# Kernel tuning notes

Hardware: AMD Instinct MI355X
Metric: run time of the kernel (lower is better)

Reference implementation:

```python
import jax, jax.numpy as jnp
import numpy as np

M, N = 63, 127            # parity checks x code length (BCH(127,64))
B = 256                   # base batch of codewords
NUM_SHIFTS = 4            # GL 'num_shifts'
NUM_ITERS = 3             # GL 'num_iterations'
PENALTY = 2.0             # GL 'penalty_weight'
BIG = 1e30

_POS = (2 * np.arange(N)) % N          # Frobenius automorphism i -> 2i mod n
_INV = np.zeros(N, np.int32); _INV[_POS] = np.arange(N)
_STEP = N // NUM_SHIFTS
_SHIFTS = [i * _STEP for i in range(NUM_SHIFTS)]  # deterministic (offset=0)


def setup_inputs() -> dict:
    key = jax.random.key(0)
    k1, k2 = jax.random.split(key)
    soft_input = jax.random.normal(k1, (B, N), dtype=jnp.float32)
    labels = jax.random.randint(k2, (B, N), 0, 2).astype(jnp.int32)
    rng = np.random.default_rng(0)
    Hnp = (rng.random((M, N)) < 0.25).astype(np.float32)
    rows = np.arange(M)
    Hnp[rows, rows % N] = 1.0              # guarantee >=2 ones per check row
    Hnp[rows, (rows + 1) % N] = 1.0
    H = jnp.asarray(Hnp, jnp.float32)
    check_weight = jnp.array([0.421], jnp.float32)
    return {"soft_input": soft_input, "labels": labels, "H": H,
            "check_weight": check_weight}


def _interleave(a, b):
    m, n1 = a.shape
    n2 = b.shape[1]
    if n1 == n2:
        return jnp.stack([a, b], axis=2).reshape(m, n1 + n2)
    inter = jnp.stack([a[:, :n2], b], axis=2).reshape(m, 2 * n2)
    return jnp.concatenate([inter, a[:, n2:]], axis=1)


def _compute_cv(vc, H, check_weight):
    # vc: [Bs, M, N] masked variable->check messages
    sign = jnp.sign((1.0 - H)[None] + vc)
    row_sign = jnp.prod(sign, axis=2, keepdims=True)      # product over row
    result_sign = row_sign * H * sign                     # extrinsic sign
    back = jnp.where(H == 0, -BIG - 1.0, 0.0)[None]
    vabs = jnp.clip(jnp.abs(vc), 0.0, BIG)
    top2 = jax.lax.top_k(-vabs + back, 2)[0]              # [Bs, M, 2]
    min1 = -top2[..., 0:1] * H                            # per-check min
    min2 = -top2[..., 1:2] * H                            # per-check 2nd min
    result = jnp.where(vabs > min1, min1, min2)           # extrinsic min
    return jax.nn.softplus(check_weight) * result * jax.lax.stop_gradient(result_sign)


def _iteration(soft, H, check_weight):
    # build super batch: [orig ; even/odd split ; frobenius perm] x rolled copies
    split = jnp.concatenate([soft[:, 0::2], soft[:, 1::2]], axis=1)
    perm = soft[:, _POS]
    base = jnp.concatenate([soft, split, perm], axis=0)   # [3B, N]
    sup = jnp.concatenate([jnp.roll(base, s, axis=1) for s in _SHIFTS], axis=0)
    vc = sup[:, None, :] * H[None]                        # [3B*S, M, N]
    cv = _compute_cv(vc, H, check_weight)
    temp = jnp.sum(cv, axis=1)                            # [3B*S, N]
    bs = 3 * B
    chunks = [jnp.roll(temp[i * bs:(i + 1) * bs], -_SHIFTS[i], axis=1)
              for i in range(NUM_SHIFTS)]
    t1 = sum(c[:B] for c in chunks)
    t2 = sum(c[B:2 * B] for c in chunks)
    width = (N + 1) // 2
    inter = _interleave(t2[:, :width], t2[:, width:])
    t3 = sum(c[2 * B:] for c in chunks)
    p = t3[:, _INV]                                       # inverse Frobenius
    return soft + (t1 + inter + p) / (3.0 * NUM_SHIFTS)


def _loss(soft, labels_f):
    weight = jnp.where(jnp.sign(soft) != 1.0 - 2.0 * labels_f, PENALTY, 1.0)
    z = -soft
    ce = jnp.maximum(z, 0.0) - z * labels_f + jnp.log1p(jnp.exp(-jnp.abs(z)))
    return jnp.sum(weight * ce)


def reference(soft_input, labels, H, check_weight):
    labels_f = labels.astype(jnp.float32)
    soft = soft_input
    outs = [soft]
    loss = jnp.float32(0.0)
    for _ in range(NUM_ITERS):
        soft = _iteration(soft, H, check_weight)
        outs.append(soft)
        loss = _loss(soft, labels_f)
    return jnp.stack(outs, axis=0), loss
```

## Files before the change

### kernel.cpp

```cpp
#include <hip/hip_runtime.h>
#include <math.h>

#define MM 63
#define NN 127
#define BB 256
#define NIT 3
#define CSRB 64
#define CSCB 44
#define PQS 65

__global__ __launch_bounds__(1024)
void decode_kernel(const float* __restrict__ soft_in,
                   const int* __restrict__ labels,
                   const float* __restrict__ Hg,
                   const float* __restrict__ cw,
                   float* __restrict__ out)
{
    const int b   = blockIdx.x;
    const int tid = threadIdx.x;

    __shared__ unsigned char csr[MM][CSRB];
    __shared__ unsigned char csc[NN][CSCB];
    __shared__ int   rcnt[MM], ccnt[NN];
    __shared__ float base0[NN + 1];
    __shared__ float2 pq[8 * PQS];
    __shared__ float red2[2];

    {
        unsigned int* w1 = (unsigned int*)&csr[0][0];
        for (int i = tid; i < MM * CSRB / 4; i += 1024) w1[i] = 0x7f7f7f7fu;
        unsigned int* w2 = (unsigned int*)&csc[0][0];
        for (int i = tid; i < NN * CSCB / 4; i += 1024) w2[i] = 0x3f3f3f3fu;
    }
    if (tid < MM) rcnt[tid] = 0;
    if (tid < NN) ccnt[tid] = 0;
    if (tid < NN) {
        float v = soft_in[b * NN + tid];
        base0[tid] = v;
        out[b * NN + tid] = v;
    }
    if (tid == NN) base0[NN] = 1e30f;
    if (tid >= 512 && tid < 520)
        pq[(tid - 512) * PQS + 63] = make_float2(0.0f, 0.0f);
    const float spw = log1pf(expf(cw[0]));
    __syncthreads();

    for (int i = tid; i < MM * NN; i += 1024) {
        if (Hg[i] != 0.0f) {
            int m = i / NN;
            int c = i - m * NN;
            int pr = atomicAdd(&rcnt[m], 1);
            csr[m][pr] = (unsigned char)c;
            int pc = atomicAdd(&ccnt[c], 1);
            csc[c][pc] = (unsigned char)m;
        }
    }
    __syncthreads();

    unsigned int aw[8];
    int aH2 = 0, aPQ = 0;
    {
        const int vs    = tid >> 7;
        const int mslot = (tid >> 1) & 63;
        const int half  = tid & 1;
        #pragma unroll
        for (int e = 0; e < 8; ++e) aw[e] = 0x7f7f7f7fu;
        if (mslot < MM) {
            const int v     = vs >> 2;
            const int shift = (vs & 3) * 31;
            const int cnt   = rcnt[mslot];
            aH2 = (cnt + 7) >> 3;
            aPQ = vs * PQS + mslot;
            const unsigned int* wp = (const unsigned int*)&csr[mslot][0];
            #pragma unroll
            for (int e = 0; e < 8; ++e) {
                if (e < aH2) {
                    unsigned int w = wp[half * aH2 + e];
                    unsigned int o = 0;
                    #pragma unroll
                    for (int j = 0; j < 4; ++j) {
                        int c = (w >> (8 * j)) & 255;
                        int t = c - shift; t += (t < 0) ? NN : 0;
                        if (v) { t <<= 1; t -= (t >= NN) ? NN : 0; }
                        t = (c == 127) ? 127 : t;
                        o |= (unsigned int)t << (8 * j);
                    }
                    aw[e] = o;
                }
            }
        }
    }

    unsigned int bw[11];
    int bC2 = 0, bn = 0, bDouble = 0;
    const float2* bPqs = pq;
    {
        const int n = tid >> 3;
        const int k = tid & 7;
        #pragma unroll
        for (int e = 0; e < 11; ++e) bw[e] = 0x3f3f3f3fu;
        if (n < NN) {
            const int v = k >> 2;
            const int s = k & 3;
            int p0 = v ? ((n * 64) % NN) : n;
            int j = p0 + s * 31; j -= (j >= NN) ? NN : 0;
            bC2 = (ccnt[j] + 3) >> 2;
            bn = n; bDouble = v;
            bPqs = &pq[((v << 2) | s) * PQS];
            const unsigned int* cwp = (const unsigned int*)&csc[j][0];
            #pragma unroll
            for (int e = 0; e < 11; ++e)
                if (e < bC2) bw[e] = cwp[e];
        }
    }

    for (int it = 0; it < NIT; ++it) {
        if (aH2 > 0) {
            float m1 = 1e30f, m2 = 1e30f;
            unsigned int sb = 0u;
            #pragma unroll
            for (int e = 0; e < 8; ++e) {
                if (e < aH2) {
                    unsigned int w = aw[e];
                    #pragma unroll
                    for (int j = 0; j < 4; ++j) {
                        int idx = (w >> (8 * j)) & 255;
                        float x = base0[idx];
                        float a = __uint_as_float(__float_as_uint(x) & 0x7fffffffu);
                        sb ^= __float_as_uint(x);
                        m2 = fminf(m2, fmaxf(a, m1));
                        m1 = fminf(m1, a);
                    }
                }
            }
            float om1 = __shfl_xor(m1, 1);
            float om2 = __shfl_xor(m2, 1);
            unsigned int osb = (unsigned int)__shfl_xor((int)sb, 1);
            float mm2 = fminf(fminf(m2, om2), fmaxf(m1, om1));
            float mm1 = fminf(m1, om1);
            sb ^= osb;
            float rs = (sb & 0x80000000u) ? -1.0f : 1.0f;
            rs = (mm1 == 0.0f) ? 0.0f : rs;
            if ((tid & 1) == 0)
                pq[aPQ] = make_float2(rs * mm1, rs * mm2);
        }
        __syncthreads();

        if (bC2 > 0) {
            const float x = base0[bn];
            const float a = fabsf(x);
            float acc = 0.0f;
            #pragma unroll
            for (int e = 0; e < 11; ++e) {
                if (e < bC2) {
                    unsigned int w = bw[e];
                    #pragma unroll
                    for (int j = 0; j < 4; ++j) {
                        int m = (w >> (8 * j)) & 255;
                        float2 pv = bPqs[m];
                        acc += (a > fabsf(pv.x)) ? pv.x : pv.y;
                    }
                }
            }
            if (bDouble) acc += acc;
            acc += __shfl_xor(acc, 1);
            acc += __shfl_xor(acc, 2);
            acc += __shfl_xor(acc, 4);
            if ((tid & 7) == 0) {
                float sx = (x > 0.0f) ? 1.0f : ((x < 0.0f) ? -1.0f : 0.0f);
                float ns = x + spw * sx * acc * (1.0f / 12.0f);
                base0[bn] = ns;
                out[(size_t)(it + 1) * (BB * NN) + b * NN + bn] = ns;
            }
        }
        __syncthreads();
    }

    float term = 0.0f;
    if (tid < NN) {
        float sft = base0[tid];
        float lf  = (float)labels[b * NN + tid];
        float sg  = (sft > 0.0f) ? 1.0f : ((sft < 0.0f) ? -1.0f : 0.0f);
        float w   = (sg != (1.0f - 2.0f * lf)) ? 2.0f : 1.0f;
        float z   = -sft;
        term = w * (fmaxf(z, 0.0f) - z * lf + log1pf(expf(-fabsf(z))));
    }
    if (tid < 128) {
        #pragma unroll
        for (int off = 32; off > 0; off >>= 1)
            term += __shfl_down(term, off);
        if ((tid & 63) == 0) red2[tid >> 6] = term;
    }
    __syncthreads();
    if (tid == 0) atomicAdd(&out[4 * BB * NN], red2[0] + red2[1]);
}

extern "C" void kernel_launch(void* const* d_in, const int* in_sizes, int n_in,
                              void* d_out, int out_size, void* d_ws, size_t ws_size,
                              hipStream_t stream) {
    const float* soft   = (const float*)d_in[0];
    const int*   labels = (const int*)  d_in[1];
    const float* H      = (const float*)d_in[2];
    const float* cw     = (const float*)d_in[3];
    float* outp = (float*)d_out;

    hipMemsetAsync(outp + 4 * BB * NN, 0, sizeof(float), stream);
    decode_kernel<<<BB, 1024, 0, stream>>>(soft, labels, H, cw, outp);
}
```

Baseline: 82.17 us.

## Precompute byte-offset gather lists and balance column work across lanes

Replaces the 8-bit index lists with precomputed 16-bit byte offsets into shared memory for both the check-node and variable-node phases. The variable-phase work is rebalanced: each column's 8 lanes now share a flattened list of 28 entries per lane instead of one list per shift and variant. The check phase splits its min tracking into two chains for more instruction-level parallelism. Per-iteration global writes are buffered in shared memory and written once at the end, and the label load is hoisted. The cost is an extra setup pass with its own barrier and more shared memory per block.

```diff
diff --git a/kernel.cpp b/kernel.cpp
--- a/kernel.cpp
+++ b/kernel.cpp
@@ -5,9 +5,12 @@
 #define NN 127
 #define BB 256
 #define NIT 3
-#define CSRB 64
+#define CSRB 68
 #define CSCB 44
 #define PQS 65
+#define WLV 112
+#define WLN (2*WLV)
+#define BCH 28
 
 __global__ __launch_bounds__(1024)
 void decode_kernel(const float* __restrict__ soft_in,
@@ -22,26 +25,28 @@
     __shared__ unsigned char csr[MM][CSRB];
     __shared__ unsigned char csc[NN][CSCB];
     __shared__ int   rcnt[MM], ccnt[NN];
-    __shared__ float base0[NN + 1];
-    __shared__ float2 pq[8 * PQS];
+    __shared__ float base0[128];
+    __shared__ float2 pqf[8 * PQS];
+    __shared__ unsigned short wl[NN * WLN];
+    __shared__ float hist[NIT][NN];
     __shared__ float red2[2];
 
     {
-        unsigned int* w1 = (unsigned int*)&csr[0][0];
-        for (int i = tid; i < MM * CSRB / 4; i += 1024) w1[i] = 0x7f7f7f7fu;
-        unsigned int* w2 = (unsigned int*)&csc[0][0];
-        for (int i = tid; i < NN * CSCB / 4; i += 1024) w2[i] = 0x3f3f3f3fu;
+        unsigned int* wlw = (unsigned int*)wl;
+        for (int i = tid; i < NN * WLN / 2; i += 1024)
+            wlw[i] = 0x01F801F8u;
     }
     if (tid < MM) rcnt[tid] = 0;
     if (tid < NN) ccnt[tid] = 0;
+    float lf = 0.0f;
     if (tid < NN) {
         float v = soft_in[b * NN + tid];
         base0[tid] = v;
         out[b * NN + tid] = v;
-    }
-    if (tid == NN) base0[NN] = 1e30f;
-    if (tid >= 512 && tid < 520)
-        pq[(tid - 512) * PQS + 63] = make_float2(0.0f, 0.0f);
+        lf = (float)labels[b * NN + tid];
+    }
+    if (tid == NN)  base0[127] = 1e30f;
+    if (tid == 128) pqf[63] = make_float2(0.0f, 0.0f);
     const float spw = log1pf(expf(cw[0]));
     __syncthreads();
 
@@ -49,137 +54,148 @@
         if (Hg[i] != 0.0f) {
             int m = i / NN;
             int c = i - m * NN;
-            int pr = atomicAdd(&rcnt[m], 1);
-            csr[m][pr] = (unsigned char)c;
-            int pc = atomicAdd(&ccnt[c], 1);
-            csc[c][pc] = (unsigned char)m;
-        }
-    }
-    __syncthreads();
-
-    unsigned int aw[8];
-    int aH2 = 0, aPQ = 0;
+            csr[m][atomicAdd(&rcnt[m], 1)] = (unsigned char)c;
+            csc[c][atomicAdd(&ccnt[c], 1)] = (unsigned char)m;
+        }
+    }
+    __syncthreads();
+
+    if (tid < NN * 8) {
+        const int n = tid >> 3, v = (tid >> 2) & 1, s = tid & 3;
+        const int p0 = v ? (n * 64) % NN : n;
+        int off = n * WLN + v * WLV;
+        for (int s2 = 0; s2 < s; ++s2) {
+            int j2 = p0 + 31 * s2; if (j2 >= NN) j2 -= NN;
+            off += ccnt[j2];
+        }
+        int j = p0 + 31 * s; if (j >= NN) j -= NN;
+        const int cc = ccnt[j];
+        const int gb = ((v * 4 + s) * PQS) * 8;
+        for (int i = 0; i < cc; ++i)
+            wl[off + i] = (unsigned short)(gb + csc[j][i] * 8);
+    }
+    __syncthreads();
+
+    unsigned int apk[16];
+    int aW = 0, pqslot = 0;
     {
-        const int vs    = tid >> 7;
-        const int mslot = (tid >> 1) & 63;
-        const int half  = tid & 1;
+        const int vs = tid >> 7, mslot = (tid >> 1) & 63, half = tid & 1;
+        if (mslot < MM) {
+            const int v = vs >> 2, shift = (vs & 3) * 31;
+            const int cnt   = rcnt[mslot];
+            const int hcnt  = (cnt + 1) >> 1;
+            const int start = half ? hcnt : 0;
+            const int mycnt = half ? (cnt - hcnt) : hcnt;
+            aW = (mycnt + 3) >> 2;
+            pqslot = vs * PQS + mslot;
+            #pragma unroll
+            for (int g = 0; g < 8; ++g) {
+                unsigned int w0 = 0x01FC01FCu, w1 = 0x01FC01FCu;
+                if (g < aW) {
+                    unsigned int ad[4];
+                    #pragma unroll
+                    for (int jj = 0; jj < 4; ++jj) {
+                        int e = 4 * g + jj;
+                        int addr = 508;
+                        if (e < mycnt) {
+                            int c = csr[mslot][start + e];
+                            int t = c - shift; t += (t < 0) ? NN : 0;
+                            if (v) { t <<= 1; t -= (t >= NN) ? NN : 0; }
+                            addr = t * 4;
+                        }
+                        ad[jj] = (unsigned int)addr;
+                    }
+                    w0 = ad[0] | (ad[1] << 16);
+                    w1 = ad[2] | (ad[3] << 16);
+                }
+                apk[2 * g] = w0; apk[2 * g + 1] = w1;
+            }
+        }
+    }
+
+    unsigned int bpk[14];
+    const int bn = tid >> 3, bk = tid & 7;
+    if (bn < NN) {
+        const unsigned int* src = (const unsigned int*)(wl + bn * WLN + bk * BCH);
         #pragma unroll
-        for (int e = 0; e < 8; ++e) aw[e] = 0x7f7f7f7fu;
-        if (mslot < MM) {
-            const int v     = vs >> 2;
-            const int shift = (vs & 3) * 31;
-            const int cnt   = rcnt[mslot];
-            aH2 = (cnt + 7) >> 3;
-            aPQ = vs * PQS + mslot;
-            const unsigned int* wp = (const unsigned int*)&csr[mslot][0];
-            #pragma unroll
-            for (int e = 0; e < 8; ++e) {
-                if (e < aH2) {
-                    unsigned int w = wp[half * aH2 + e];
-                    unsigned int o = 0;
-                    #pragma unroll
-                    for (int j = 0; j < 4; ++j) {
-                        int c = (w >> (8 * j)) & 255;
-                        int t = c - shift; t += (t < 0) ? NN : 0;
-                        if (v) { t <<= 1; t -= (t >= NN) ? NN : 0; }
-                        t = (c == 127) ? 127 : t;
-                        o |= (unsigned int)t << (8 * j);
-                    }
-                    aw[e] = o;
-                }
-            }
-        }
-    }
-
-    unsigned int bw[11];
-    int bC2 = 0, bn = 0, bDouble = 0;
-    const float2* bPqs = pq;
-    {
-        const int n = tid >> 3;
-        const int k = tid & 7;
+        for (int i = 0; i < 14; ++i) bpk[i] = src[i];
+    } else {
         #pragma unroll
-        for (int e = 0; e < 11; ++e) bw[e] = 0x3f3f3f3fu;
-        if (n < NN) {
-            const int v = k >> 2;
-            const int s = k & 3;
-            int p0 = v ? ((n * 64) % NN) : n;
-            int j = p0 + s * 31; j -= (j >= NN) ? NN : 0;
-            bC2 = (ccnt[j] + 3) >> 2;
-            bn = n; bDouble = v;
-            bPqs = &pq[((v << 2) | s) * PQS];
-            const unsigned int* cwp = (const unsigned int*)&csc[j][0];
-            #pragma unroll
-            for (int e = 0; e < 11; ++e)
-                if (e < bC2) bw[e] = cwp[e];
-        }
-    }
+        for (int i = 0; i < 14; ++i) bpk[i] = 0x01F801F8u;
+    }
+
+    const float f12 = spw * (1.0f / 12.0f);
 
     for (int it = 0; it < NIT; ++it) {
-        if (aH2 > 0) {
-            float m1 = 1e30f, m2 = 1e30f;
+        if (aW > 0) {
+            float m1a = 1e30f, m2a = 1e30f, m1b = 1e30f, m2b = 1e30f;
             unsigned int sb = 0u;
             #pragma unroll
-            for (int e = 0; e < 8; ++e) {
-                if (e < aH2) {
-                    unsigned int w = aw[e];
-                    #pragma unroll
-                    for (int j = 0; j < 4; ++j) {
-                        int idx = (w >> (8 * j)) & 255;
-                        float x = base0[idx];
-                        float a = __uint_as_float(__float_as_uint(x) & 0x7fffffffu);
-                        sb ^= __float_as_uint(x);
-                        m2 = fminf(m2, fmaxf(a, m1));
-                        m1 = fminf(m1, a);
-                    }
+            for (int g = 0; g < 8; ++g) {
+                if (g < aW) {
+                    unsigned int w0 = apk[2 * g], w1 = apk[2 * g + 1];
+                    float x0 = *(const float*)((const char*)base0 + (w0 & 0xffffu));
+                    float x1 = *(const float*)((const char*)base0 + (w0 >> 16));
+                    float x2 = *(const float*)((const char*)base0 + (w1 & 0xffffu));
+                    float x3 = *(const float*)((const char*)base0 + (w1 >> 16));
+                    sb ^= __float_as_uint(x0) ^ __float_as_uint(x1)
+                        ^ __float_as_uint(x2) ^ __float_as_uint(x3);
+                    float a0 = fabsf(x0), a1 = fabsf(x1);
+                    float a2 = fabsf(x2), a3 = fabsf(x3);
+                    m2a = fminf(m2a, fmaxf(a0, m1a)); m1a = fminf(m1a, a0);
+                    m2b = fminf(m2b, fmaxf(a1, m1b)); m1b = fminf(m1b, a1);
+                    m2a = fminf(m2a, fmaxf(a2, m1a)); m1a = fminf(m1a, a2);
+                    m2b = fminf(m2b, fmaxf(a3, m1b)); m1b = fminf(m1b, a3);
                 }
             }
+            float m1 = fminf(m1a, m1b);
+            float m2 = fminf(fminf(m2a, m2b), fmaxf(m1a, m1b));
             float om1 = __shfl_xor(m1, 1);
             float om2 = __shfl_xor(m2, 1);
             unsigned int osb = (unsigned int)__shfl_xor((int)sb, 1);
+            float mm1 = fminf(m1, om1);
             float mm2 = fminf(fminf(m2, om2), fmaxf(m1, om1));
-            float mm1 = fminf(m1, om1);
             sb ^= osb;
             float rs = (sb & 0x80000000u) ? -1.0f : 1.0f;
             rs = (mm1 == 0.0f) ? 0.0f : rs;
-            if ((tid & 1) == 0)
-                pq[aPQ] = make_float2(rs * mm1, rs * mm2);
+            if ((tid & 1) == 0) pqf[pqslot] = make_float2(rs * mm1, rs * mm2);
         }
         __syncthreads();
 
-        if (bC2 > 0) {
+        if (bn < NN) {
             const float x = base0[bn];
-            const float a = fabsf(x);
             float acc = 0.0f;
             #pragma unroll
-            for (int e = 0; e < 11; ++e) {
-                if (e < bC2) {
-                    unsigned int w = bw[e];
-                    #pragma unroll
-                    for (int j = 0; j < 4; ++j) {
-                        int m = (w >> (8 * j)) & 255;
-                        float2 pv = bPqs[m];
-                        acc += (a > fabsf(pv.x)) ? pv.x : pv.y;
-                    }
-                }
-            }
-            if (bDouble) acc += acc;
+            for (int i = 0; i < 14; ++i) {
+                unsigned int w = bpk[i];
+                float2 p0 = *(const float2*)((const char*)pqf + (w & 0xffffu));
+                float2 p1 = *(const float2*)((const char*)pqf + (w >> 16));
+                acc += (fabsf(x) > fabsf(p0.x)) ? p0.x : p0.y;
+                acc += (fabsf(x) > fabsf(p1.x)) ? p1.x : p1.y;
+            }
+            if (bk >= 4) acc += acc;
             acc += __shfl_xor(acc, 1);
             acc += __shfl_xor(acc, 2);
             acc += __shfl_xor(acc, 4);
-            if ((tid & 7) == 0) {
+            if (bk == 0) {
                 float sx = (x > 0.0f) ? 1.0f : ((x < 0.0f) ? -1.0f : 0.0f);
-                float ns = x + spw * sx * acc * (1.0f / 12.0f);
+                float ns = fmaf(f12 * sx, acc, x);
                 base0[bn] = ns;
-                out[(size_t)(it + 1) * (BB * NN) + b * NN + bn] = ns;
+                hist[it][bn] = ns;
             }
         }
         __syncthreads();
+    }
+
+    if (tid < NIT * NN) {
+        int itx = tid / NN;
+        int n   = tid - itx * NN;
+        out[(size_t)(itx + 1) * (BB * NN) + b * NN + n] = hist[itx][n];
     }
 
     float term = 0.0f;
     if (tid < NN) {
         float sft = base0[tid];
-        float lf  = (float)labels[b * NN + tid];
         float sg  = (sft > 0.0f) ? 1.0f : ((sft < 0.0f) ? -1.0f : 0.0f);
         float w   = (sg != (1.0f - 2.0f * lf)) ? 2.0f : 1.0f;
         float z   = -sft;
@@ -187,8 +203,7 @@
     }
     if (tid < 128) {
         #pragma unroll
-        for (int off = 32; off > 0; off >>= 1)
-            term += __shfl_down(term, off);
+        for (int off = 32; off > 0; off >>= 1) term += __shfl_down(term, off);
         if ((tid & 63) == 0) red2[tid >> 6] = term;
     }
     __syncthreads();
```

Result: slower. 85.48 us (+4.0%).
